# Optimization experiments

Measured on AMD Instinct MI355X. Metric: run time of the kernel, lower is better.

The kernel has to match this reference:

```python
import jax, jax.numpy as jnp
import numpy as np

D = 3            # input_ch (pos dims)
L = 16           # n_levels
F = 2            # n_feats per level
LOG2 = 19
CAP = 1 << LOG2  # hashmap capacity per level
COARSEST, FINEST = 16.0, 2048.0
N = 524288
D1 = D + 1
HASH_MULT = np.int32(2531011)


def _elevate_matrix():
    # Linear map R^D -> hyperplane {sum=0} in R^{D+1} (Adams et al. permutohedral lattice)
    sf = 1.0 / np.sqrt(np.arange(1, D + 1, dtype=np.float64) * np.arange(2, D + 2, dtype=np.float64))
    E = np.zeros((D1, D), np.float32)
    E[0, :] = sf
    for i in range(1, D1):
        E[i, i - 1] = -i * sf[i - 1]
        E[i, i:] = sf[i:]
    return E


def _scales():
    g = (FINEST / COARSEST) ** (np.arange(L, dtype=np.float64) / (L - 1))
    return (COARSEST * g).astype(np.float32)


def permuto_forward(pos, params):
    E = jnp.asarray(_elevate_matrix())
    scales = jnp.asarray(_scales())
    x = pos[None] * scales[:, None, None]              # [L,N,D]
    elev = jnp.einsum('vp,lnp->lnv', E, x)             # [L,N,D1]
    # nearest lattice remainder-0 point (multiples of D1)
    rem0f = jnp.round(elev / D1) * D1
    sums = (jnp.sum(rem0f, -1) / D1).astype(jnp.int32)  # exactly integer
    di = elev - rem0f
    # rank[i] = #{j : d_j > d_i  or (d_j == d_i and j < i)}
    gt = di[..., None, :] > di[..., :, None]
    eq = di[..., None, :] == di[..., :, None]
    jlt = jnp.arange(D1)[None, :] < jnp.arange(D1)[:, None]
    rank = jnp.sum(gt | (eq & jlt), -1).astype(jnp.int32) + sums[..., None]
    rem0 = rem0f.astype(jnp.int32)
    under = (rank < 0).astype(jnp.int32)
    over = (rank > D).astype(jnp.int32)
    rank = rank + (under - over) * D1
    rem0 = rem0 + (under - over) * D1
    # barycentric weights of the D1 simplex vertices
    delta = (elev - rem0.astype(elev.dtype)) / D1      # [L,N,D1]
    dbr = jnp.take_along_axis(delta, jnp.argsort(rank, -1), -1)  # delta ordered by rank
    w0 = 1.0 + dbr[..., -1] - dbr[..., 0]
    w = jnp.concatenate([w0[..., None], -(dbr[..., 1:] - dbr[..., :-1])[..., ::-1]], -1)  # [L,N,D1]
    # integer keys of the D1 simplex vertices (first D coords; last is implicit)
    kk = jnp.arange(D1, dtype=jnp.int32)
    keys = (rem0[..., None, :D] + kk[:, None]
            - D1 * (rank[..., None, :D] > (D - kk[:, None])).astype(jnp.int32))  # [L,N,D1,D]
    # hash: k = (k + key_i) * 2531011, wrap in 32 bits, mask to capacity (pow2)
    h = jnp.zeros(keys.shape[:-1], jnp.int32)
    for i in range(D):
        h = (h + keys[..., i]) * HASH_MULT
    idx = h & (CAP - 1)                                # [L,N,D1]
    flat_idx = idx + jnp.arange(L, dtype=jnp.int32)[:, None, None] * CAP
    feats = params.reshape(L * CAP, F)[flat_idx]       # [L,N,D1,F]
    out = jnp.einsum('lnv,lnvf->lnf', w, feats)        # [L,N,F]
    return jnp.moveaxis(out, 0, 1).reshape(pos.shape[0], L * F)


def setup_inputs() -> dict:
    key = jax.random.key(0)
    k1, k2 = jax.random.split(key)
    pos = jax.random.uniform(k1, (N, D), jnp.float32)                 # coords in [0,1)
    params = jax.random.normal(k2, (L * CAP * F,), jnp.float32) * 1e-4  # param_init std
    return {"input": pos, "flattened_params": params}


def reference(input, flattened_params):
    return permuto_forward(input, flattened_params)
```

## Files before the change

### kernel.cpp

```cpp
#include <hip/hip_runtime.h>
#include <hip/hip_fp16.h>
#include <cmath>

namespace {

typedef float    vf4 __attribute__((ext_vector_type(4)));
typedef unsigned uv2 __attribute__((ext_vector_type(2)));

constexpr int kN = 524288;
constexpr int kL = 16;
constexpr int kCapLog2 = 19;
constexpr int kCap = 1 << kCapLog2;
constexpr int kCapMask = kCap - 1;
constexpr unsigned kHashMult = 2531011u;

constexpr int cD[4][3]   = {{ 8, 8, 6},{10,10, 9},{13,12,10},{17,16,14}};
constexpr int cB[4][3]   = {{-4,-16,-16},{-4,-20,-24},{-4,-24,-28},{-4,-32,-40}};
constexpr int cOff[4]    = {0, 1536, 5136, 11376};
constexpr int kDenseCnt  = 26608;

constexpr int kMegaMain  = 15360;
constexpr int kBuildBlks = 104;
constexpr int kConvBaseF4 = 7 * (kCap * 2 / 4);

constexpr int kPB        = kN / 256;
constexpr int kFinePrim  = 8 * kPB;
constexpr int kFineTail  = kPB;
constexpr int kCoarseBlk = kPB;

struct ScaleArr { float s[kL]; };

__device__ __forceinline__ void permuto_point(
    float x0, float x1, float x2, int rem0[4], int rank[4], float w[4])
{
    const float E00 = (float)( 0.70710678118654752440);
    const float E01 = (float)( 0.40824829046386301637);
    const float E02 = (float)( 0.28867513459481288225);
    const float E10 = (float)(-0.70710678118654752440);
    const float E21 = (float)(-2.0 * 0.40824829046386301637);
    const float E32 = (float)(-3.0 * 0.28867513459481288225);

    float elev[4];
    elev[0] = E00 * x0 + E01 * x1 + E02 * x2;
    elev[1] = E10 * x0 + E01 * x1 + E02 * x2;
    elev[2] =            E21 * x1 + E02 * x2;
    elev[3] =                       E32 * x2;

    float rem0f[4], di[4];
    #pragma unroll
    for (int v = 0; v < 4; ++v) {
        rem0f[v] = rintf(elev[v] * 0.25f) * 4.0f;
        di[v]    = elev[v] - rem0f[v];
    }
    const int sums = (int)((((rem0f[0] + rem0f[1]) + rem0f[2]) + rem0f[3]) * 0.25f);

    #pragma unroll
    for (int a = 0; a < 4; ++a) {
        int r = 0;
        #pragma unroll
        for (int b = 0; b < 4; ++b)
            r += (di[b] > di[a]) || (di[b] == di[a] && b < a);
        rank[a] = r + sums;
        rem0[a] = (int)rem0f[a];
    }
    #pragma unroll
    for (int v = 0; v < 4; ++v) {
        if (rank[v] < 0)      { rank[v] += 4; rem0[v] += 4; }
        else if (rank[v] > 3) { rank[v] -= 4; rem0[v] -= 4; }
    }

    float dbr[4];
    #pragma unroll
    for (int v = 0; v < 4; ++v)
        dbr[rank[v] & 3] = (elev[v] - (float)rem0[v]) * 0.25f;

    w[0] = (1.0f + dbr[3]) - dbr[0];
    w[1] = dbr[2] - dbr[3];
    w[2] = dbr[1] - dbr[2];
    w[3] = dbr[0] - dbr[1];
}

__device__ __forceinline__ void fine_job(
    const float* __restrict__ pos, const unsigned* __restrict__ tab,
    unsigned* __restrict__ out_t16, const ScaleArr& sc, int level, int n)
{
    const float s  = sc.s[level];
    const float x0 = __builtin_nontemporal_load(pos + 3 * n + 0) * s;
    const float x1 = __builtin_nontemporal_load(pos + 3 * n + 1) * s;
    const float x2 = __builtin_nontemporal_load(pos + 3 * n + 2) * s;

    int rem0[4], rank[4];
    float w[4];
    permuto_point(x0, x1, x2, rem0, rank, w);

    const unsigned* __restrict__ t = tab + ((size_t)level << kCapLog2);
    int hidx[4];
    #pragma unroll
    for (int k = 0; k < 4; ++k) {
        int h = 0;
        #pragma unroll
        for (int i = 0; i < 3; ++i) {
            const int key = rem0[i] + k - 4 * (rank[i] > 3 - k);
            h = (int)((unsigned)(h + key) * kHashMult);
        }
        hidx[k] = h & kCapMask;
    }
    unsigned e[4];
    #pragma unroll
    for (int k = 0; k < 4; ++k) e[k] = t[hidx[k]];

    float o0 = 0.0f, o1 = 0.0f;
    #pragma unroll
    for (int k = 0; k < 4; ++k) {
        const __half2 hv = *reinterpret_cast<const __half2*>(&e[k]);
        o0 += w[k] * __low2float(hv);
        o1 += w[k] * __high2float(hv);
    }
    const __half2 po = __floats2half2_rn(o0, o1);
    __builtin_nontemporal_store(*reinterpret_cast<const unsigned*>(&po),
                                out_t16 + ((size_t)level << kCapLog2) + n);
}

__global__ __launch_bounds__(256) void mega1(
    const float* __restrict__ pos,
    const float* __restrict__ params,
    unsigned* __restrict__ tab,
    unsigned* __restrict__ out_t16,
    unsigned* __restrict__ dense,
    ScaleArr sc)
{
    const int b = blockIdx.x;
    if (b < kMegaMain) {
        const int q = b / 5, r = b % 5;
        if (r < 2) {
            const int idx   = q * 2 + r;
            const int level = 4 + (idx >> 11);
            const int n     = ((idx & 2047) << 8) + threadIdx.x;

            const float s  = sc.s[level];
            const float x0 = __builtin_nontemporal_load(pos + 3 * n + 0) * s;
            const float x1 = __builtin_nontemporal_load(pos + 3 * n + 1) * s;
            const float x2 = __builtin_nontemporal_load(pos + 3 * n + 2) * s;

            int rem0[4], rank[4];
            float w[4];
            permuto_point(x0, x1, x2, rem0, rank, w);

            const float2* __restrict__ t2 =
                (const float2*)params + ((size_t)level << kCapLog2);
            int hidx[4];
            #pragma unroll
            for (int k = 0; k < 4; ++k) {
                int h = 0;
                #pragma unroll
                for (int i = 0; i < 3; ++i) {
                    const int key = rem0[i] + k - 4 * (rank[i] > 3 - k);
                    h = (int)((unsigned)(h + key) * kHashMult);
                }
                hidx[k] = h & kCapMask;
            }
            float2 f[4];
            #pragma unroll
            for (int k = 0; k < 4; ++k) f[k] = t2[hidx[k]];

            float o0 = 0.0f, o1 = 0.0f;
            #pragma unroll
            for (int k = 0; k < 4; ++k) { o0 += w[k] * f[k].x; o1 += w[k] * f[k].y; }

            const __half2 po = __floats2half2_rn(o0, o1);
            __builtin_nontemporal_store(*reinterpret_cast<const unsigned*>(&po),
                                        out_t16 + ((size_t)level << kCapLog2) + n);
        } else {
            const int i  = q * 3 + (r - 2);
            const int jj = kConvBaseF4 + i * 256 + threadIdx.x;
            vf4 v = __builtin_nontemporal_load((const vf4*)params + jj);
            __half2 a = __floats2half2_rn(v.x, v.y);
            __half2 c = __floats2half2_rn(v.z, v.w);
            uv2 o;
            o.x = *reinterpret_cast<unsigned*>(&a);
            o.y = *reinterpret_cast<unsigned*>(&c);
            __builtin_nontemporal_store(o, (uv2*)tab + jj);
        }
    } else {
        const int e = (b - kMegaMain) * 256 + threadIdx.x;
        if (e >= kDenseCnt) return;
        int l, r;
        if      (e < cOff[1]) { l = 0; r = e; }
        else if (e < cOff[2]) { l = 1; r = e - cOff[1]; }
        else if (e < cOff[3]) { l = 2; r = e - cOff[2]; }
        else                  { l = 3; r = e - cOff[3]; }
        const int d0 = cD[l][0], d1 = cD[l][1], d2 = cD[l][2];
        const int per = d0 * d1 * d2;
        int rr = r;
        const int k  = rr / per;  rr -= k * per;
        const int i0 = rr / (d1 * d2); rr -= i0 * (d1 * d2);
        const int i1 = rr / d2;
        const int i2 = rr - i1 * d2;

        const int key0 = cB[l][0] + 4 * i0 + k;
        const int key1 = cB[l][1] + 4 * i1 + k;
        const int key2 = cB[l][2] + 4 * i2 + k;
        int h = 0;
        h = (int)((unsigned)(h + key0) * kHashMult);
        h = (int)((unsigned)(h + key1) * kHashMult);
        h = (int)((unsigned)(h + key2) * kHashMult);
        const size_t entry = ((size_t)l << kCapLog2) + (h & kCapMask);
        const __half2 hv = __floats2half2_rn(params[entry * 2], params[entry * 2 + 1]);
        dense[e] = *reinterpret_cast<const unsigned*>(&hv);
    }
}

__global__ __launch_bounds__(256, 8) void fine715c(
    const float* __restrict__ pos,
    const unsigned* __restrict__ tab,
    const unsigned* __restrict__ dense,
    unsigned* __restrict__ out_t16,
    ScaleArr sc)
{
    const int b = blockIdx.x;

    if (b < kFinePrim) {
        const int level = 7 + (b & 7);
        const int n = ((b >> 3) << 8) + threadIdx.x;
        fine_job(pos, tab, out_t16, sc, level, n);
    } else if (b < kFinePrim + kFineTail) {
        const int q = b - kFinePrim;
        const int c = (q >> 3) + ((q & 7) << 8);
        const int n = (c << 8) + threadIdx.x;
        fine_job(pos, tab, out_t16, sc, 15, n);
    } else {
        const int n = (b - kFinePrim - kFineTail) * 256 + threadIdx.x;
        const float p0 = __builtin_nontemporal_load(pos + 3 * n + 0);
        const float p1 = __builtin_nontemporal_load(pos + 3 * n + 1);
        const float p2 = __builtin_nontemporal_load(pos + 3 * n + 2);

        #pragma unroll 1
        for (int l = 0; l < 4; ++l) {
            const float s = sc.s[l];
            int rem0[4], rank[4];
            float w[4];
            permuto_point(p0 * s, p1 * s, p2 * s, rem0, rank, w);

            const unsigned* __restrict__ dl = dense + cOff[l];
            unsigned ev[4];
            #pragma unroll
            for (int k = 0; k < 4; ++k) {
                const int i0 = (rem0[0] - 4 * (rank[0] > 3 - k) - cB[l][0]) >> 2;
                const int i1 = (rem0[1] - 4 * (rank[1] > 3 - k) - cB[l][1]) >> 2;
                const int i2 = (rem0[2] - 4 * (rank[2] > 3 - k) - cB[l][2]) >> 2;
                ev[k] = dl[((k * cD[l][0] + i0) * cD[l][1] + i1) * cD[l][2] + i2];
            }
            float o0 = 0.0f, o1 = 0.0f;
            #pragma unroll
            for (int k = 0; k < 4; ++k) {
                const __half2 hv = *reinterpret_cast<const __half2*>(&ev[k]);
                o0 += w[k] * __low2float(hv);
                o1 += w[k] * __high2float(hv);
            }
            const __half2 po = __floats2half2_rn(o0, o1);
            __builtin_nontemporal_store(*reinterpret_cast<const unsigned*>(&po),
                                        out_t16 + ((size_t)l << kCapLog2) + n);
        }
    }
}

__global__ __launch_bounds__(256) void transpose16(
    const unsigned* __restrict__ out_t16, vf4* __restrict__ out4)
{
    __shared__ unsigned tile[256][17];
    const int t  = threadIdx.x;
    const int p0 = blockIdx.x * 256;

    #pragma unroll
    for (int l = 0; l < kL; ++l)
        tile[t][l] = __builtin_nontemporal_load(out_t16 + ((size_t)l << kCapLog2) + p0 + t);
    __syncthreads();

    const size_t base = (size_t)p0 * 8;
    #pragma unroll
    for (int j = 0; j < 4; ++j) {
        const int idx = j * 256 + t;
        const int p = idx >> 2, q = idx & 3;
        float f[8];
        #pragma unroll
        for (int i = 0; i < 4; ++i) {
            const unsigned u = tile[p][4 * q + i];
            const __half2 hv = *reinterpret_cast<const __half2*>(&u);
            f[2 * i + 0] = __low2float(hv);
            f[2 * i + 1] = __high2float(hv);
        }
        vf4 a, c;
        a.x = f[0]; a.y = f[1]; a.z = f[2]; a.w = f[3];
        c.x = f[4]; c.y = f[5]; c.z = f[6]; c.w = f[7];
        out4[base + (size_t)p * 8 + 2 * q + 0] = a;
        out4[base + (size_t)p * 8 + 2 * q + 1] = c;
    }
}

__global__ __launch_bounds__(256) void permuto_fwd(
    const float* __restrict__ pos,
    const float* __restrict__ params,
    float* __restrict__ out,
    ScaleArr sc)
{
    const int gid = blockIdx.x * 256 + threadIdx.x;
    const int l = gid & (kL - 1);
    const int n = gid >> 4;

    const float s  = sc.s[l];
    const float x0 = pos[3 * n + 0] * s;
    const float x1 = pos[3 * n + 1] * s;
    const float x2 = pos[3 * n + 2] * s;

    int rem0[4], rank[4];
    float w[4];
    permuto_point(x0, x1, x2, rem0, rank, w);

    const float2* __restrict__ tab = (const float2*)params + ((size_t)l << kCapLog2);
    float o0 = 0.0f, o1 = 0.0f;
    #pragma unroll
    for (int k = 0; k < 4; ++k) {
        int h = 0;
        #pragma unroll
        for (int i = 0; i < 3; ++i) {
            const int key = rem0[i] + k - 4 * (rank[i] > 3 - k);
            h = (int)((unsigned)(h + key) * kHashMult);
        }
        const float2 f = tab[h & kCapMask];
        o0 += w[k] * f.x;
        o1 += w[k] * f.y;
    }
    ((float2*)out)[(n << 4) + l] = make_float2(o0, o1);
}

}

extern "C" void kernel_launch(void* const* d_in, const int* in_sizes, int n_in,
                              void* d_out, int out_size, void* d_ws, size_t ws_size,
                              hipStream_t stream) {
    const float* pos    = (const float*)d_in[0];
    const float* params = (const float*)d_in[1];
    float* out          = (float*)d_out;

    ScaleArr sc;
    for (int l = 0; l < kL; ++l)
        sc.s[l] = (float)(16.0 * pow(128.0, (double)l / 15.0));

    const size_t tab_bytes   = (size_t)kL * kCap * 4;
    const size_t outt_bytes  = (size_t)kL * kN * 4;
    const size_t dense_bytes = (size_t)kDenseCnt * 4;

    if (ws_size >= tab_bytes + outt_bytes + dense_bytes) {
        unsigned* tab     = (unsigned*)d_ws;
        unsigned* out_t16 = (unsigned*)((char*)d_ws + tab_bytes);
        unsigned* dense   = (unsigned*)((char*)d_ws + tab_bytes + outt_bytes);

        mega1<<<kMegaMain + kBuildBlks, 256, 0, stream>>>(pos, params, tab, out_t16, dense, sc);
        fine715c<<<kFinePrim + kFineTail + kCoarseBlk, 256, 0, stream>>>(pos, tab, dense, out_t16, sc);
        transpose16<<<kN / 256, 256, 0, stream>>>(out_t16, (vf4*)out);
    } else {
        permuto_fwd<<<(kN * kL) / 256, 256, 0, stream>>>(pos, params, out, sc);
    }
}
```

Measured before the change: 168.5 us.

## Split fine gather into two halves and overlap first-half transpose with second-half gather

Splits the fine-level gather into two kernels, each covering half the points. The first kernel also runs the coarse levels for all points. The second kernel gathers the fine levels for the second half while other blocks transpose the first half's results, and a final small kernel transposes the second half. The goal is to overlap the bandwidth-bound transpose with the latency-bound random gathers, at the cost of an extra launch and a shared-memory tile allocated in every gatherB block, which may lower occupancy for the gather blocks.

```diff
diff --git a/kernel.cpp b/kernel.cpp
--- a/kernel.cpp
+++ b/kernel.cpp
@@ -14,6 +14,10 @@
 constexpr int kCapMask = kCap - 1;
 constexpr unsigned kHashMult = 2531011u;
 
+constexpr int kHalf = kN / 2;
+constexpr int kHB   = kHalf / 256;
+constexpr int kPB   = kN / 256;
+
 constexpr int cD[4][3]   = {{ 8, 8, 6},{10,10, 9},{13,12,10},{17,16,14}};
 constexpr int cB[4][3]   = {{-4,-16,-16},{-4,-20,-24},{-4,-24,-28},{-4,-32,-40}};
 constexpr int cOff[4]    = {0, 1536, 5136, 11376};
@@ -22,11 +26,6 @@
 constexpr int kMegaMain  = 15360;
 constexpr int kBuildBlks = 104;
 constexpr int kConvBaseF4 = 7 * (kCap * 2 / 4);
-
-constexpr int kPB        = kN / 256;
-constexpr int kFinePrim  = 8 * kPB;
-constexpr int kFineTail  = kPB;
-constexpr int kCoarseBlk = kPB;
 
 struct ScaleArr { float s[kL]; };
 
@@ -119,6 +118,76 @@
     const __half2 po = __floats2half2_rn(o0, o1);
     __builtin_nontemporal_store(*reinterpret_cast<const unsigned*>(&po),
                                 out_t16 + ((size_t)level << kCapLog2) + n);
+}
+
+__device__ __forceinline__ void coarse_job(
+    const float* __restrict__ pos, const unsigned* __restrict__ dense,
+    unsigned* __restrict__ out_t16, const ScaleArr& sc, int n)
+{
+    const float p0 = __builtin_nontemporal_load(pos + 3 * n + 0);
+    const float p1 = __builtin_nontemporal_load(pos + 3 * n + 1);
+    const float p2 = __builtin_nontemporal_load(pos + 3 * n + 2);
+
+    #pragma unroll 1
+    for (int l = 0; l < 4; ++l) {
+        const float s = sc.s[l];
+        int rem0[4], rank[4];
+        float w[4];
+        permuto_point(p0 * s, p1 * s, p2 * s, rem0, rank, w);
+
+        const unsigned* __restrict__ dl = dense + cOff[l];
+        unsigned ev[4];
+        #pragma unroll
+        for (int k = 0; k < 4; ++k) {
+            const int i0 = (rem0[0] - 4 * (rank[0] > 3 - k) - cB[l][0]) >> 2;
+            const int i1 = (rem0[1] - 4 * (rank[1] > 3 - k) - cB[l][1]) >> 2;
+            const int i2 = (rem0[2] - 4 * (rank[2] > 3 - k) - cB[l][2]) >> 2;
+            ev[k] = dl[((k * cD[l][0] + i0) * cD[l][1] + i1) * cD[l][2] + i2];
+        }
+        float o0 = 0.0f, o1 = 0.0f;
+        #pragma unroll
+        for (int k = 0; k < 4; ++k) {
+            const __half2 hv = *reinterpret_cast<const __half2*>(&ev[k]);
+            o0 += w[k] * __low2float(hv);
+            o1 += w[k] * __high2float(hv);
+        }
+        const __half2 po = __floats2half2_rn(o0, o1);
+        __builtin_nontemporal_store(*reinterpret_cast<const unsigned*>(&po),
+                                    out_t16 + ((size_t)l << kCapLog2) + n);
+    }
+}
+
+__device__ __forceinline__ void transpose_job(
+    const unsigned* __restrict__ out_t16, vf4* __restrict__ out4,
+    int pb, unsigned (*tile)[17])
+{
+    const int t  = threadIdx.x;
+    const int p0 = pb * 256;
+
+    #pragma unroll
+    for (int l = 0; l < kL; ++l)
+        tile[t][l] = __builtin_nontemporal_load(out_t16 + ((size_t)l << kCapLog2) + p0 + t);
+    __syncthreads();
+
+    const size_t base = (size_t)p0 * 8;
+    #pragma unroll
+    for (int j = 0; j < 4; ++j) {
+        const int idx = j * 256 + t;
+        const int p = idx >> 2, q = idx & 3;
+        float f[8];
+        #pragma unroll
+        for (int i = 0; i < 4; ++i) {
+            const unsigned u = tile[p][4 * q + i];
+            const __half2 hv = *reinterpret_cast<const __half2*>(&u);
+            f[2 * i + 0] = __low2float(hv);
+            f[2 * i + 1] = __high2float(hv);
+        }
+        vf4 a, c;
+        a.x = f[0]; a.y = f[1]; a.z = f[2]; a.w = f[3];
+        c.x = f[4]; c.y = f[5]; c.z = f[6]; c.w = f[7];
+        out4[base + (size_t)p * 8 + 2 * q + 0] = a;
+        out4[base + (size_t)p * 8 + 2 * q + 1] = c;
+    }
 }
 
 __global__ __launch_bounds__(256) void mega1(
@@ -210,7 +279,7 @@
     }
 }
 
-__global__ __launch_bounds__(256, 8) void fine715c(
+__global__ __launch_bounds__(256, 8) void gatherA(
     const float* __restrict__ pos,
     const unsigned* __restrict__ tab,
     const unsigned* __restrict__ dense,
@@ -218,83 +287,49 @@
     ScaleArr sc)
 {
     const int b = blockIdx.x;
-
-    if (b < kFinePrim) {
+    if (b < 8 * kHB) {
         const int level = 7 + (b & 7);
         const int n = ((b >> 3) << 8) + threadIdx.x;
         fine_job(pos, tab, out_t16, sc, level, n);
-    } else if (b < kFinePrim + kFineTail) {
-        const int q = b - kFinePrim;
-        const int c = (q >> 3) + ((q & 7) << 8);
+    } else if (b < 9 * kHB) {
+        const int q = b - 8 * kHB;
+        const int c = (q >> 3) + ((q & 7) << 7);
         const int n = (c << 8) + threadIdx.x;
         fine_job(pos, tab, out_t16, sc, 15, n);
     } else {
-        const int n = (b - kFinePrim - kFineTail) * 256 + threadIdx.x;
-        const float p0 = __builtin_nontemporal_load(pos + 3 * n + 0);
-        const float p1 = __builtin_nontemporal_load(pos + 3 * n + 1);
-        const float p2 = __builtin_nontemporal_load(pos + 3 * n + 2);
-
-        #pragma unroll 1
-        for (int l = 0; l < 4; ++l) {
-            const float s = sc.s[l];
-            int rem0[4], rank[4];
-            float w[4];
-            permuto_point(p0 * s, p1 * s, p2 * s, rem0, rank, w);
-
-            const unsigned* __restrict__ dl = dense + cOff[l];
-            unsigned ev[4];
-            #pragma unroll
-            for (int k = 0; k < 4; ++k) {
-                const int i0 = (rem0[0] - 4 * (rank[0] > 3 - k) - cB[l][0]) >> 2;
-                const int i1 = (rem0[1] - 4 * (rank[1] > 3 - k) - cB[l][1]) >> 2;
-                const int i2 = (rem0[2] - 4 * (rank[2] > 3 - k) - cB[l][2]) >> 2;
-                ev[k] = dl[((k * cD[l][0] + i0) * cD[l][1] + i1) * cD[l][2] + i2];
-            }
-            float o0 = 0.0f, o1 = 0.0f;
-            #pragma unroll
-            for (int k = 0; k < 4; ++k) {
-                const __half2 hv = *reinterpret_cast<const __half2*>(&ev[k]);
-                o0 += w[k] * __low2float(hv);
-                o1 += w[k] * __high2float(hv);
-            }
-            const __half2 po = __floats2half2_rn(o0, o1);
-            __builtin_nontemporal_store(*reinterpret_cast<const unsigned*>(&po),
-                                        out_t16 + ((size_t)l << kCapLog2) + n);
-        }
-    }
-}
-
-__global__ __launch_bounds__(256) void transpose16(
+        coarse_job(pos, dense, out_t16, sc, (b - 9 * kHB) * 256 + threadIdx.x);
+    }
+}
+
+__global__ __launch_bounds__(256, 8) void gatherB(
+    const float* __restrict__ pos,
+    const unsigned* __restrict__ tab,
+    const unsigned* __restrict__ out_t16c,
+    unsigned* __restrict__ out_t16,
+    vf4* __restrict__ out4,
+    ScaleArr sc)
+{
+    __shared__ unsigned tile[256][17];
+    const int b = blockIdx.x;
+    if (b < 8 * kHB) {
+        const int level = 7 + (b & 7);
+        const int n = kHalf + ((b >> 3) << 8) + threadIdx.x;
+        fine_job(pos, tab, out_t16, sc, level, n);
+    } else if (b < 9 * kHB) {
+        const int q = b - 8 * kHB;
+        const int c = (q >> 3) + ((q & 7) << 7);
+        const int n = kHalf + (c << 8) + threadIdx.x;
+        fine_job(pos, tab, out_t16, sc, 15, n);
+    } else {
+        transpose_job(out_t16c, out4, b - 9 * kHB, tile);
+    }
+}
+
+__global__ __launch_bounds__(256) void transposeB(
     const unsigned* __restrict__ out_t16, vf4* __restrict__ out4)
 {
     __shared__ unsigned tile[256][17];
-    const int t  = threadIdx.x;
-    const int p0 = blockIdx.x * 256;
-
-    #pragma unroll
-    for (int l = 0; l < kL; ++l)
-        tile[t][l] = __builtin_nontemporal_load(out_t16 + ((size_t)l << kCapLog2) + p0 + t);
-    __syncthreads();
-
-    const size_t base = (size_t)p0 * 8;
-    #pragma unroll
-    for (int j = 0; j < 4; ++j) {
-        const int idx = j * 256 + t;
-        const int p = idx >> 2, q = idx & 3;
-        float f[8];
-        #pragma unroll
-        for (int i = 0; i < 4; ++i) {
-            const unsigned u = tile[p][4 * q + i];
-            const __half2 hv = *reinterpret_cast<const __half2*>(&u);
-            f[2 * i + 0] = __low2float(hv);
-            f[2 * i + 1] = __high2float(hv);
-        }
-        vf4 a, c;
-        a.x = f[0]; a.y = f[1]; a.z = f[2]; a.w = f[3];
-        c.x = f[4]; c.y = f[5]; c.z = f[6]; c.w = f[7];
-        out4[base + (size_t)p * 8 + 2 * q + 0] = a;
-        out4[base + (size_t)p * 8 + 2 * q + 1] = c;
-    }
+    transpose_job(out_t16, out4, blockIdx.x + kHB, tile);
 }
 
 __global__ __launch_bounds__(256) void permuto_fwd(
@@ -356,8 +391,9 @@
         unsigned* dense   = (unsigned*)((char*)d_ws + tab_bytes + outt_bytes);
 
         mega1<<<kMegaMain + kBuildBlks, 256, 0, stream>>>(pos, params, tab, out_t16, dense, sc);
-        fine715c<<<kFinePrim + kFineTail + kCoarseBlk, 256, 0, stream>>>(pos, tab, dense, out_t16, sc);
-        transpose16<<<kN / 256, 256, 0, stream>>>(out_t16, (vf4*)out);
+        gatherA<<<9 * kHB + kPB, 256, 0, stream>>>(pos, tab, dense, out_t16, sc);
+        gatherB<<<9 * kHB + kHB, 256, 0, stream>>>(pos, tab, out_t16, out_t16, (vf4*)out, sc);
+        transposeB<<<kHB, 256, 0, stream>>>(out_t16, (vf4*)out);
     } else {
         permuto_fwd<<<(kN * kL) / 256, 256, 0, stream>>>(pos, params, out, sc);
     }
```

After: 171.5 us. No clear change (+1.7%).
